# Kernel optimization log

Measured on AMD Instinct MI355X. Metric: run time of the kernel, lower is better.

## Reference

```python
import jax, jax.numpy as jnp
import numpy as np

N, D, H, W = 16, 3, 160, 160
M, K, P = 8, 10, 15


def setup_inputs() -> dict:
    key = jax.random.key(0)
    ks = jax.random.split(key, 7)
    pm = (P - 1) // 2
    T = jax.random.normal(ks[0], (N, D, H, W), dtype=jnp.float32)
    # offsets must keep floor(d) in [-pm, pm-1] so padded gathers stay in-bounds
    u = lambda k: jax.random.uniform(k, (M, K), dtype=jnp.float32,
                                     minval=-float(pm), maxval=float(pm - 1))
    dx1, dx2, dy1, dy2 = u(ks[1]), u(ks[2]), u(ks[3]), u(ks[4])
    th = jax.random.uniform(ks[5], (M, K), dtype=jnp.float32, minval=-0.5, maxval=0.5)
    # ambiguity thresholds per fern: row 0 = positive, row 1 = negative
    amb = jnp.stack([jnp.full((M, K), 0.2, jnp.float32),
                     jnp.full((M, K), -0.2, jnp.float32)], axis=1)  # (M, 2, K)
    channels = jnp.tile(jnp.arange(D, dtype=jnp.int32), (K + D - 1) // D)[:K]
    return {"T": T, "dx1": dx1, "dx2": dx2, "dy1": dy1, "dy2": dy2,
            "th": th, "amb": amb, "channels": channels, "patch_size": P}


def _fern_bits(T, dx1, dx2, dy1, dy2, th, amb, channels, patch_size):
    Nn, Dn, Hn, Wn = T.shape
    pm = (patch_size - 1) // 2              # patch_middle
    outH = Hn - patch_size + 1
    outW = Wn - patch_size + 1
    # ZeroPad2d((0,1,0,1)): pad one zero on right and bottom (for bilinear +1 neighbor)
    Tpad = jnp.pad(T, ((0, 0), (0, 0), (0, 1), (0, 1)))
    Mn, Kn = dx1.shape
    MK = Mn * Kn
    ch = jnp.tile(channels, Mn)             # (MK,) m-major, k-minor channel per bit fn
    ry = jnp.arange(outH)
    rx = jnp.arange(outW)

    def sample(dx, dy):
        # bilinear interpolation of every output pixel at offset (dy, dx), all MK at once
        dx = dx.reshape(-1)
        dy = dy.reshape(-1)
        fx = jnp.abs(dx - jnp.floor(dx))    # (MK,) fractional parts (differentiable)
        fy = jnp.abs(dy - jnp.floor(dy))
        sx = (pm + jnp.floor(dx)).astype(jnp.int32)   # (MK,) integer slice starts
        sy = (pm + jnp.floor(dy)).astype(jnp.int32)
        iy = sy[:, None] + ry               # (MK, outH)
        ix = sx[:, None] + rx               # (MK, outW)
        chb = ch[:, None, None]

        def g(oy, ox):                      # corner gather -> (N, MK, outH, outW)
            return Tpad[:, chb, (iy + oy)[:, :, None], (ix + ox)[:, None, :]]

        fxb = fx[:, None, None]
        fyb = fy[:, None, None]
        return ((1 - fyb) * ((1 - fxb) * g(0, 0) + fxb * g(0, 1))
                + fyb * ((1 - fxb) * g(1, 0) + fxb * g(1, 1)))

    P1 = sample(dx1, dy1)
    P2 = sample(dx2, dy2)
    temp = P1 - P2
    temp = jnp.where(jnp.abs(temp) < 1e-5, 0.0, temp)   # zero-out near-ties
    b = temp - th.reshape(1, MK, 1, 1)
    pos = amb[:, 0, :].reshape(1, MK, 1, 1)
    neg = amb[:, 1, :].reshape(1, MK, 1, 1)
    # B = clamp((b - neg) / (pos - neg + eps), 0, 1)
    return jnp.clip((b - neg) / (pos - neg + 1e-29), 0.0, 1.0)


def reference(T, dx1, dx2, dy1, dy2, th, amb, channels, patch_size):
    return _fern_bits(T, dx1, dx2, dy1, dy2, th, amb, channels, patch_size)
```

## Files before the change

### kernel.cpp

```cpp
#include <hip/hip_runtime.h>

#define NN   16
#define DD   3
#define HH   160
#define WW   160
#define MM   8
#define KK   10
#define PP   15
#define PM   7
#define OUTH 146
#define OUTW 146
#define MK   (MM*KK)
#define YT   73
#define XT   37
#define UNITS (YT*XT)

typedef float vfloat2 __attribute__((ext_vector_type(2)));

__global__ __launch_bounds__(256)
void fern_bits_kernel(const float* __restrict__ T,
                      const float* __restrict__ dx1,
                      const float* __restrict__ dx2,
                      const float* __restrict__ dy1,
                      const float* __restrict__ dy2,
                      const float* __restrict__ th,
                      const float* __restrict__ amb,
                      const int*   __restrict__ channels,
                      float* __restrict__ out)
{
    const int mk = blockIdx.y;
    const int n  = blockIdx.z;
    const int k  = mk % KK;
    const int m  = mk / KK;
    const int c  = channels[k];

    float a, f;
    a = dx1[mk]; f = floorf(a); const float fx1 = a - f; const int sx1 = PM + (int)f;
    a = dy1[mk]; f = floorf(a); const float fy1 = a - f; const int sy1 = PM + (int)f;
    a = dx2[mk]; f = floorf(a); const float fx2 = a - f; const int sx2 = PM + (int)f;
    a = dy2[mk]; f = floorf(a); const float fy2 = a - f; const int sy2 = PM + (int)f;
    const float thv = th[mk];
    const float pos = amb[(m*2 + 0)*KK + k];
    const float neg = amb[(m*2 + 1)*KK + k];
    const float scl = 1.0f / (pos - neg + 1e-29f);

    const float* __restrict__ Tp = T + (size_t)(n*DD + c) * (HH*WW);

    const int u = blockIdx.x * 256 + threadIdx.x;
    if (u >= UNITS) return;
    const int ty = u / XT;
    const int tx = u - ty * XT;
    const int y  = ty * 2;
    int x = tx * 4;
    if (x > OUTW - 4) x = OUTW - 4;

    const float* r1 = Tp + (sy1 + y) * WW + (sx1 + x);
    const float* r2 = Tp + (sy2 + y) * WW + (sx2 + x);

    float v1v[3][5], v2v[3][5];
#pragma unroll
    for (int j = 0; j < 3; ++j) {
#pragma unroll
        for (int i = 0; i < 5; ++i) {
            v1v[j][i] = r1[j * WW + i];
            v2v[j][i] = r2[j * WW + i];
        }
    }

    float h1[3][4], h2[3][4];
#pragma unroll
    for (int j = 0; j < 3; ++j) {
#pragma unroll
        for (int i = 0; i < 4; ++i) {
            h1[j][i] = v1v[j][i] + fx1 * (v1v[j][i+1] - v1v[j][i]);
            h2[j][i] = v2v[j][i] + fx2 * (v2v[j][i+1] - v2v[j][i]);
        }
    }

    float q1a[4], q1b[4], q2a[4], q2b[4];
#pragma unroll
    for (int i = 0; i < 4; ++i) {
        q1a[i] = h1[0][i] + fy1 * (h1[1][i] - h1[0][i]);
        q1b[i] = h1[1][i] + fy1 * (h1[2][i] - h1[1][i]);
        q2a[i] = h2[0][i] + fy2 * (h2[1][i] - h2[0][i]);
        q2b[i] = h2[1][i] + fy2 * (h2[2][i] - h2[1][i]);
    }

    float o0[4], o1[4];
#pragma unroll
    for (int i = 0; i < 4; ++i) {
        float d0 = q1a[i] - q2a[i]; if (fabsf(d0) < 1e-5f) d0 = 0.0f;
        float d1 = q1b[i] - q2b[i]; if (fabsf(d1) < 1e-5f) d1 = 0.0f;
        o0[i] = __builtin_amdgcn_fmed3f((d0 - thv - neg) * scl, 0.0f, 1.0f);
        o1[i] = __builtin_amdgcn_fmed3f((d1 - thv - neg) * scl, 0.0f, 1.0f);
    }

    float* orow0 = out + ((size_t)(n * MK + mk) * OUTH + y) * OUTW + x;
    float* orow1 = orow0 + OUTW;
    vfloat2 s;
    s.x = o0[0]; s.y = o0[1]; __builtin_nontemporal_store(s, (vfloat2*)(orow0));
    s.x = o0[2]; s.y = o0[3]; __builtin_nontemporal_store(s, (vfloat2*)(orow0 + 2));
    s.x = o1[0]; s.y = o1[1]; __builtin_nontemporal_store(s, (vfloat2*)(orow1));
    s.x = o1[2]; s.y = o1[3]; __builtin_nontemporal_store(s, (vfloat2*)(orow1 + 2));
}

extern "C" void kernel_launch(void* const* d_in, const int* in_sizes, int n_in,
                              void* d_out, int out_size, void* d_ws, size_t ws_size,
                              hipStream_t stream) {
    const float* T        = (const float*)d_in[0];
    const float* dx1      = (const float*)d_in[1];
    const float* dx2      = (const float*)d_in[2];
    const float* dy1      = (const float*)d_in[3];
    const float* dy2      = (const float*)d_in[4];
    const float* th       = (const float*)d_in[5];
    const float* amb      = (const float*)d_in[6];
    const int*   channels = (const int*)d_in[7];
    float* out = (float*)d_out;

    dim3 grid((UNITS + 255) / 256, MK, NN);
    dim3 block(256, 1, 1);
    fern_bits_kernel<<<grid, block, 0, stream>>>(T, dx1, dx2, dy1, dy2, th, amb,
                                                 channels, out);
}
```

Before: 151.4 us.

## Stage input row tiles in LDS and loop over bit functions per block

```diff
diff --git a/kernel.cpp b/kernel.cpp
--- a/kernel.cpp
+++ b/kernel.cpp
@@ -11,13 +11,21 @@
 #define OUTH 146
 #define OUTW 146
 #define MK   (MM*KK)
-#define YT   73
-#define XT   37
-#define UNITS (YT*XT)
+
+#define BY      10
+#define ROWS    23
+#define NTILES  15
+#define SGRP    4
+#define MKG     20
+#define THREADS 384
+#define CPW     73
+#define RGRP    5
+#define PLANE   (HH*WW)
+#define STAGE4  (DD*ROWS*(WW/4))
 
 typedef float vfloat2 __attribute__((ext_vector_type(2)));
 
-__global__ __launch_bounds__(256)
+__global__ __launch_bounds__(THREADS)
 void fern_bits_kernel(const float* __restrict__ T,
                       const float* __restrict__ dx1,
                       const float* __restrict__ dx2,
@@ -28,80 +36,89 @@
                       const int*   __restrict__ channels,
                       float* __restrict__ out)
 {
-    const int mk = blockIdx.y;
-    const int n  = blockIdx.z;
-    const int k  = mk % KK;
-    const int m  = mk / KK;
-    const int c  = channels[k];
+    __shared__ float lds[DD * ROWS * WW];
 
-    float a, f;
-    a = dx1[mk]; f = floorf(a); const float fx1 = a - f; const int sx1 = PM + (int)f;
-    a = dy1[mk]; f = floorf(a); const float fy1 = a - f; const int sy1 = PM + (int)f;
-    a = dx2[mk]; f = floorf(a); const float fx2 = a - f; const int sx2 = PM + (int)f;
-    a = dy2[mk]; f = floorf(a); const float fy2 = a - f; const int sy2 = PM + (int)f;
-    const float thv = th[mk];
-    const float pos = amb[(m*2 + 0)*KK + k];
-    const float neg = amb[(m*2 + 1)*KK + k];
-    const float scl = 1.0f / (pos - neg + 1e-29f);
+    const int tid = threadIdx.x;
+    const int n   = blockIdx.z;
+    const int y0  = min((int)blockIdx.x * BY, OUTH - BY);
 
-    const float* __restrict__ Tp = T + (size_t)(n*DD + c) * (HH*WW);
+    const float* __restrict__ Tn = T + (size_t)n * DD * PLANE;
+#pragma unroll 2
+    for (int j = tid; j < STAGE4; j += THREADS) {
+        const int c   = j / (ROWS * (WW/4));
+        const int rem = j - c * (ROWS * (WW/4));
+        const int r   = rem / (WW/4);
+        const int q   = rem - r * (WW/4);
+        const float4 v = *(const float4*)(Tn + c * PLANE + (y0 + r) * WW + q * 4);
+        *(float4*)&lds[(c * ROWS + r) * WW + q * 4] = v;
+    }
+    __syncthreads();
 
-    const int u = blockIdx.x * 256 + threadIdx.x;
-    if (u >= UNITS) return;
-    const int ty = u / XT;
-    const int tx = u - ty * XT;
-    const int y  = ty * 2;
-    int x = tx * 4;
-    if (x > OUTW - 4) x = OUTW - 4;
+    const int cp = tid % CPW;
+    const int rg = tid / CPW;
+    const bool active = (rg < RGRP);
+    const int xo  = cp * 2;
+    const int ro0 = rg * 2;
 
-    const float* r1 = Tp + (sy1 + y) * WW + (sx1 + x);
-    const float* r2 = Tp + (sy2 + y) * WW + (sx2 + x);
+    float* __restrict__ obase =
+        out + ((size_t)(n * MK + blockIdx.y * MKG) * OUTH + (y0 + ro0)) * OUTW + xo;
 
-    float v1v[3][5], v2v[3][5];
-#pragma unroll
-    for (int j = 0; j < 3; ++j) {
-#pragma unroll
-        for (int i = 0; i < 5; ++i) {
-            v1v[j][i] = r1[j * WW + i];
-            v2v[j][i] = r2[j * WW + i];
+    for (int g = 0; g < MKG; ++g) {
+        const int mk = blockIdx.y * MKG + g;
+        const int k  = mk % KK;
+        const int m  = mk / KK;
+        const int c  = channels[k];
+
+        float a, f;
+        a = dx1[mk]; f = floorf(a); const float fx1 = a - f; const int sx1 = PM + (int)f;
+        a = dy1[mk]; f = floorf(a); const float fy1 = a - f; const int sy1 = PM + (int)f;
+        a = dx2[mk]; f = floorf(a); const float fx2 = a - f; const int sx2 = PM + (int)f;
+        a = dy2[mk]; f = floorf(a); const float fy2 = a - f; const int sy2 = PM + (int)f;
+        const float thv = th[mk];
+        const float pos = amb[(m*2 + 0)*KK + k];
+        const float neg = amb[(m*2 + 1)*KK + k];
+        const float scl = 1.0f / (pos - neg + 1e-29f);
+
+        if (active) {
+            const int b1 = (c * ROWS + ro0 + sy1) * WW + xo + sx1;
+            const float t00 = lds[b1      ], t01 = lds[b1 + 1      ], t02 = lds[b1 + 2      ];
+            const float t10 = lds[b1 + WW ], t11 = lds[b1 + WW + 1 ], t12 = lds[b1 + WW + 2 ];
+            const float t20 = lds[b1 + 2*WW], t21 = lds[b1 + 2*WW + 1], t22 = lds[b1 + 2*WW + 2];
+            const float h00 = t00 + fx1 * (t01 - t00), h01 = t01 + fx1 * (t02 - t01);
+            const float h10 = t10 + fx1 * (t11 - t10), h11 = t11 + fx1 * (t12 - t11);
+            const float h20 = t20 + fx1 * (t21 - t20), h21 = t21 + fx1 * (t22 - t21);
+            const float p1aa = h00 + fy1 * (h10 - h00);
+            const float p1ab = h01 + fy1 * (h11 - h01);
+            const float p1ba = h10 + fy1 * (h20 - h10);
+            const float p1bb = h11 + fy1 * (h21 - h11);
+
+            const int b2 = (c * ROWS + ro0 + sy2) * WW + xo + sx2;
+            const float u00 = lds[b2      ], u01 = lds[b2 + 1      ], u02 = lds[b2 + 2      ];
+            const float u10 = lds[b2 + WW ], u11 = lds[b2 + WW + 1 ], u12 = lds[b2 + WW + 2 ];
+            const float u20 = lds[b2 + 2*WW], u21 = lds[b2 + 2*WW + 1], u22 = lds[b2 + 2*WW + 2];
+            const float g00 = u00 + fx2 * (u01 - u00), g01 = u01 + fx2 * (u02 - u01);
+            const float g10 = u10 + fx2 * (u11 - u10), g11 = u11 + fx2 * (u12 - u11);
+            const float g20 = u20 + fx2 * (u21 - u20), g21 = u21 + fx2 * (u22 - u21);
+            const float p2aa = g00 + fy2 * (g10 - g00);
+            const float p2ab = g01 + fy2 * (g11 - g01);
+            const float p2ba = g10 + fy2 * (g20 - g10);
+            const float p2bb = g11 + fy2 * (g21 - g11);
+
+            float daa = p1aa - p2aa; if (fabsf(daa) < 1e-5f) daa = 0.0f;
+            float dab = p1ab - p2ab; if (fabsf(dab) < 1e-5f) dab = 0.0f;
+            float dba = p1ba - p2ba; if (fabsf(dba) < 1e-5f) dba = 0.0f;
+            float dbb = p1bb - p2bb; if (fabsf(dbb) < 1e-5f) dbb = 0.0f;
+            const float oaa = __builtin_amdgcn_fmed3f((daa - thv - neg) * scl, 0.0f, 1.0f);
+            const float oab = __builtin_amdgcn_fmed3f((dab - thv - neg) * scl, 0.0f, 1.0f);
+            const float oba = __builtin_amdgcn_fmed3f((dba - thv - neg) * scl, 0.0f, 1.0f);
+            const float obb = __builtin_amdgcn_fmed3f((dbb - thv - neg) * scl, 0.0f, 1.0f);
+
+            float* orow = obase + (size_t)g * (OUTH * OUTW);
+            vfloat2 s;
+            s.x = oaa; s.y = oab; __builtin_nontemporal_store(s, (vfloat2*)(orow));
+            s.x = oba; s.y = obb; __builtin_nontemporal_store(s, (vfloat2*)(orow + OUTW));
         }
     }
-
-    float h1[3][4], h2[3][4];
-#pragma unroll
-    for (int j = 0; j < 3; ++j) {
-#pragma unroll
-        for (int i = 0; i < 4; ++i) {
-            h1[j][i] = v1v[j][i] + fx1 * (v1v[j][i+1] - v1v[j][i]);
-            h2[j][i] = v2v[j][i] + fx2 * (v2v[j][i+1] - v2v[j][i]);
-        }
-    }
-
-    float q1a[4], q1b[4], q2a[4], q2b[4];
-#pragma unroll
-    for (int i = 0; i < 4; ++i) {
-        q1a[i] = h1[0][i] + fy1 * (h1[1][i] - h1[0][i]);
-        q1b[i] = h1[1][i] + fy1 * (h1[2][i] - h1[1][i]);
-        q2a[i] = h2[0][i] + fy2 * (h2[1][i] - h2[0][i]);
-        q2b[i] = h2[1][i] + fy2 * (h2[2][i] - h2[1][i]);
-    }
-
-    float o0[4], o1[4];
-#pragma unroll
-    for (int i = 0; i < 4; ++i) {
-        float d0 = q1a[i] - q2a[i]; if (fabsf(d0) < 1e-5f) d0 = 0.0f;
-        float d1 = q1b[i] - q2b[i]; if (fabsf(d1) < 1e-5f) d1 = 0.0f;
-        o0[i] = __builtin_amdgcn_fmed3f((d0 - thv - neg) * scl, 0.0f, 1.0f);
-        o1[i] = __builtin_amdgcn_fmed3f((d1 - thv - neg) * scl, 0.0f, 1.0f);
-    }
-
-    float* orow0 = out + ((size_t)(n * MK + mk) * OUTH + y) * OUTW + x;
-    float* orow1 = orow0 + OUTW;
-    vfloat2 s;
-    s.x = o0[0]; s.y = o0[1]; __builtin_nontemporal_store(s, (vfloat2*)(orow0));
-    s.x = o0[2]; s.y = o0[3]; __builtin_nontemporal_store(s, (vfloat2*)(orow0 + 2));
-    s.x = o1[0]; s.y = o1[1]; __builtin_nontemporal_store(s, (vfloat2*)(orow1));
-    s.x = o1[2]; s.y = o1[3]; __builtin_nontemporal_store(s, (vfloat2*)(orow1 + 2));
 }
 
 extern "C" void kernel_launch(void* const* d_in, const int* in_sizes, int n_in,
@@ -117,8 +134,8 @@
     const int*   channels = (const int*)d_in[7];
     float* out = (float*)d_out;
 
-    dim3 grid((UNITS + 255) / 256, MK, NN);
-    dim3 block(256, 1, 1);
+    dim3 grid(NTILES, SGRP, NN);
+    dim3 block(THREADS, 1, 1);
     fern_bits_kernel<<<grid, block, 0, stream>>>(T, dx1, dx2, dy1, dy2, th, amb,
                                                  channels, out);
 }
```

After: 157.6 us. 4.1% more time.
